# Kernel tuning notes

Measured on AMD Instinct MI355X. Metric: run time of the kernel, lower is better.

The kernel has to match this reference:

```python
import jax, jax.numpy as jnp
import numpy as np

B, T, C = 2, 2048, 1024
H = 16
D = C // H
E = 16
K = 2
THETA = 10000.0
ALPHA = 0.01
EPS = 1e-5


def rmsnorm(x, w):
    ms = jnp.mean(jnp.square(x), axis=-1, keepdims=True)
    return x * jax.lax.rsqrt(ms + EPS) * w


def rope_cos_sin(t_len, dim):
    # matches precompute_freqs_cis: freqs = theta**(-2i/dim), angles = t * freqs
    freqs = 1.0 / THETA ** (jnp.arange(0, dim // 2, dtype=jnp.float32) * 2.0 / dim)
    ang = jnp.arange(t_len, dtype=jnp.float32)[:, None] * freqs[None, :]  # [T, D/2]
    return jnp.cos(ang), jnp.sin(ang)


def apply_rope(x, cos, sin):
    # x: [B,T,H,D]; complex rotation on consecutive pairs (view_as_complex semantics)
    xr = x.reshape(x.shape[:-1] + (D // 2, 2))
    x0, x1 = xr[..., 0], xr[..., 1]
    c = cos[None, :, None, :]
    s = sin[None, :, None, :]
    return jnp.stack([x0 * c - x1 * s, x0 * s + x1 * c], axis=-1).reshape(x.shape)


def mlp(x, wf, bf, wp, bp):
    return jax.nn.silu(x @ wf + bf) @ wp + bp


def setup_inputs() -> dict:
    key = jax.random.key(0)
    ks = jax.random.split(key, 16)
    s = 0.02
    return {
        'x': jax.random.normal(ks[0], (B, T, C), jnp.float32),
        'ln1_w': jax.random.normal(ks[1], (C,), jnp.float32),
        'ln2_w': jax.random.normal(ks[2], (C,), jnp.float32),
        'w_attn': jax.random.normal(ks[3], (C, 3 * C), jnp.float32) * s,
        'b_attn': jnp.zeros((3 * C,), jnp.float32),
        'w_proj': jax.random.normal(ks[4], (C, C), jnp.float32) * s,
        'b_proj': jnp.zeros((C,), jnp.float32),
        'gate_w': jax.random.normal(ks[5], (E, C), jnp.float32) * s,
        'gate_bias': jnp.zeros((E,), jnp.float32),
        'exp_wf': jax.random.normal(ks[6], (E, C, 2 * C), jnp.float32) * s,
        'exp_bf': jnp.zeros((E, 2 * C), jnp.float32),
        'exp_wp': jax.random.normal(ks[7], (E, 2 * C, C), jnp.float32) * s,
        'exp_bp': jnp.zeros((E, C), jnp.float32),
        'sh_wf': jax.random.normal(ks[8], (C, 2 * C), jnp.float32) * s,
        'sh_bf': jnp.zeros((2 * C,), jnp.float32),
        'sh_wp': jax.random.normal(ks[9], (2 * C, C), jnp.float32) * s,
        'sh_bp': jnp.zeros((C,), jnp.float32),
    }


def reference(x, ln1_w, ln2_w, w_attn, b_attn, w_proj, b_proj, gate_w, gate_bias,
              exp_wf, exp_bf, exp_wp, exp_bp, sh_wf, sh_bf, sh_wp, sh_bp):
    # ---- attention sub-block ----
    h = rmsnorm(x, ln1_w)
    qkv = h @ w_attn + b_attn  # [B,T,3C]
    q, k, v = jnp.split(qkv, 3, axis=-1)
    q = q.reshape(B, T, H, D)
    k = k.reshape(B, T, H, D)
    v = v.reshape(B, T, H, D)
    cos, sin = rope_cos_sin(T, D)
    q = apply_rope(q, cos, sin)
    k = apply_rope(k, cos, sin)
    scores = jnp.einsum('bqhd,bkhd->bhqk', q, k) / jnp.sqrt(jnp.float32(D))
    causal = jnp.tril(jnp.ones((T, T), dtype=bool))
    scores = jnp.where(causal, scores, -jnp.inf)
    attn = jax.nn.softmax(scores, axis=-1)
    y = jnp.einsum('bhqk,bkhd->bqhd', attn, v).reshape(B, T, C)
    x = x + y @ w_proj + b_proj
    # ---- MoE sub-block ----
    h = rmsnorm(x, ln2_w).reshape(-1, C)  # [N,C]
    N = h.shape[0]
    logits = h @ gate_w.T
    p = jax.nn.softmax(logits.astype(jnp.float32), axis=-1)  # original_scores [N,E]
    _, idx = jax.lax.top_k(p + gate_bias, K)  # topk on biased scores
    w_sel = jnp.take_along_axis(p, idx, axis=-1)  # weights from unbiased scores [N,K]
    onehot = jax.nn.one_hot(idx, E, dtype=p.dtype)  # [N,K,E]
    w_dense = jnp.sum(onehot * w_sel[..., None], axis=1)  # [N,E] combine weights
    counts = jnp.sum(onehot, axis=(0, 1))  # bincount
    f_i = counts * E / (K * N + 1e-6)
    expert_probs = p.mean(axis=0)
    lb_loss = ALPHA * jnp.sum(f_i * expert_probs)
    out = jnp.zeros_like(h)
    for i in range(E):  # fixed small expert count
        out = out + mlp(h, exp_wf[i], exp_bf[i], exp_wp[i], exp_bp[i]) * w_dense[:, i:i + 1]
    out = out + mlp(h, sh_wf, sh_bf, sh_wp, sh_bp)
    return x + out.reshape(B, T, C), lb_loss
```

## Files before the change

kernel.cpp:

```cpp
#include <hip/hip_runtime.h>

typedef __bf16 bf16x8 __attribute__((ext_vector_type(8)));
typedef short  short8 __attribute__((ext_vector_type(8)));
typedef float  f32x4  __attribute__((ext_vector_type(4)));
typedef unsigned short u16;

#define NTOK 4096
#define TSEQ 2048
#define CDIM 1024
#define NEXP 16

__device__ __forceinline__ u16 f2bf(float f){
  union { float f; unsigned u; } v; v.f = f;
  unsigned r = v.u + 0x7fffu + ((v.u >> 16) & 1u);
  return (u16)(r >> 16);
}
__device__ __forceinline__ float bf2f(u16 u){
  union { unsigned u; float f; } v; v.u = ((unsigned)u) << 16; return v.f;
}

__device__ __forceinline__ f32x4 mfma16(short8 a, short8 b, f32x4 c){
  return __builtin_amdgcn_mfma_f32_16x16x32_bf16(
      __builtin_bit_cast(bf16x8, a), __builtin_bit_cast(bf16x8, b), c, 0, 0, 0);
}

__device__ __forceinline__ void gload_lds16(const void* g, void* l){
  __builtin_amdgcn_global_load_lds((__attribute__((address_space(1))) void*)g,
                                   (__attribute__((address_space(3))) void*)l,
                                   16, 0, 0);
}

__device__ __forceinline__ void tp_body(const float* __restrict__ in, u16* __restrict__ out,
                                        int K, int N, int k0, int n0, u16* lds16, int tid)
{
  int tx = tid & 15;
#pragma unroll
  for (int p = 0; p < 2; ++p) {
    int q = (tid >> 4) + p * 16;
    int k = 2 * q;
    float4 v0 = *(const float4*)(in + (size_t)(k0 + k)     * N + n0 + tx * 4);
    float4 v1 = *(const float4*)(in + (size_t)(k0 + k + 1) * N + n0 + tx * 4);
    const float* a0 = (const float*)&v0;
    const float* a1 = (const float*)&v1;
#pragma unroll
    for (int i = 0; i < 4; ++i) {
      unsigned val = (unsigned)f2bf(a0[i]) | ((unsigned)f2bf(a1[i]) << 16);
      *(unsigned*)&lds16[(tx * 4 + i) * 66 + k] = val;
    }
  }
  __syncthreads();
#pragma unroll
  for (int p = 0; p < 2; ++p) {
    int n = (tid >> 3) + p * 32;
    int k8 = (tid & 7) * 8;
    const unsigned* l32 = (const unsigned*)&lds16[n * 66 + k8];
    uint4 o4;
    o4.x = l32[0]; o4.y = l32[1]; o4.z = l32[2]; o4.w = l32[3];
    *(uint4*)(out + (size_t)(n0 + n) * K + k0 + k8) = o4;
  }
}

__global__ void transpose_wattn_k(const float* __restrict__ in, u16* __restrict__ out)
{
  __shared__ u16 lds16[64 * 66];
  int r = blockIdx.x;
  int n0 = (r % 48) * 64, k0 = (r / 48) * 64;
  tp_body(in, out, 1024, 3072, k0, n0, lds16, threadIdx.x);
}

__global__ void concat_bias_k(const float* __restrict__ exp_bf, const float* __restrict__ sh_bf,
                              const float* __restrict__ exp_bp, const float* __restrict__ sh_bp,
                              float* __restrict__ bf17, float* __restrict__ bp17,
                              int* __restrict__ counts)
{
  int i = blockIdx.x * 256 + threadIdx.x;
  if (i < 16 * 2048) bf17[i] = exp_bf[i];
  else if (i < 17 * 2048) bf17[i] = sh_bf[i - 16 * 2048];
  if (i < 16 * 1024) bp17[i] = exp_bp[i];
  else if (i < 17 * 1024) bp17[i] = sh_bp[i - 16 * 1024];
  if (blockIdx.x == 0 && threadIdx.x <= NEXP)
    counts[threadIdx.x] = (threadIdx.x == NEXP) ? NTOK : 0;
}

__global__ void rmsnorm_k(const float* __restrict__ x, const float* __restrict__ w,
                          u16* __restrict__ ob)
{
  int row = blockIdx.x, tid = threadIdx.x;
  const float4* xr = (const float4*)(x + (size_t)row * CDIM);
  float4 v = xr[tid];
  float ss = v.x*v.x + v.y*v.y + v.z*v.z + v.w*v.w;
  for (int d = 1; d < 64; d <<= 1) ss += __shfl_xor(ss, d);
  __shared__ float wacc[4];
  if ((tid & 63) == 0) wacc[tid >> 6] = ss;
  __syncthreads();
  float tot = wacc[0] + wacc[1] + wacc[2] + wacc[3];
  float scale = rsqrtf(tot * (1.0f / CDIM) + 1e-5f);
  float4 wv = ((const float4*)w)[tid];
  float o0 = v.x * scale * wv.x, o1 = v.y * scale * wv.y;
  float o2 = v.z * scale * wv.z, o3 = v.w * scale * wv.w;
  ushort4 ov; ov.x = f2bf(o0); ov.y = f2bf(o1); ov.z = f2bf(o2); ov.w = f2bf(o3);
  ((ushort4*)(ob + (size_t)row * CDIM))[tid] = ov;
}

__global__ void rmsnorm_gate_k(const float* __restrict__ x2, const float* __restrict__ w,
                               const float* __restrict__ gw, const float* __restrict__ gb,
                               u16* __restrict__ ob,
                               int* __restrict__ route_e, float* __restrict__ route_w,
                               int* __restrict__ counts, float* __restrict__ probs)
{
  int row = blockIdx.x, tid = threadIdx.x;
  __shared__ float hrow[CDIM];
  __shared__ float wacc[4];
  __shared__ float part[16][17];
  __shared__ float sm[16];

  const float4* xr = (const float4*)(x2 + (size_t)row * CDIM);
  float4 v = xr[tid];
  float ss = v.x*v.x + v.y*v.y + v.z*v.z + v.w*v.w;
  for (int d = 1; d < 64; d <<= 1) ss += __shfl_xor(ss, d);
  if ((tid & 63) == 0) wacc[tid >> 6] = ss;
  __syncthreads();
  float tot = wacc[0] + wacc[1] + wacc[2] + wacc[3];
  float scale = rsqrtf(tot * (1.0f / CDIM) + 1e-5f);
  float4 wv = ((const float4*)w)[tid];
  float o0 = v.x * scale * wv.x, o1 = v.y * scale * wv.y;
  float o2 = v.z * scale * wv.z, o3 = v.w * scale * wv.w;
  ((float4*)hrow)[tid] = make_float4(o0, o1, o2, o3);
  ushort4 ov; ov.x = f2bf(o0); ov.y = f2bf(o1); ov.z = f2bf(o2); ov.w = f2bf(o3);
  ((ushort4*)(ob + (size_t)row * CDIM))[tid] = ov;
  __syncthreads();

  int e = tid & 15, seg = tid >> 4;
  const float4* gw4 = (const float4*)(gw + (size_t)e * CDIM + seg * 64);
  const float4* hs4 = (const float4*)(hrow + seg * 64);
  float p = 0.f;
#pragma unroll
  for (int i = 0; i < 16; ++i) {
    float4 gv = gw4[i];
    float4 hv = hs4[i];
    p += hv.x * gv.x;
    p += hv.y * gv.y;
    p += hv.z * gv.z;
    p += hv.w * gv.w;
  }
  part[e][seg] = p;
  __syncthreads();
  if (tid < 16) {
    float lg = 0.f;
    for (int s = 0; s < 16; ++s) lg += part[tid][s];
    sm[tid] = lg;
  }
  __syncthreads();
  if (tid == 0) {
    float mx = sm[0];
    for (int i = 1; i < 16; ++i) mx = fmaxf(mx, sm[i]);
    float ssum = 0.f;
    for (int i = 0; i < 16; ++i) { float pe = expf(sm[i] - mx); sm[i] = pe; ssum += pe; }
    float inv = 1.0f / ssum;
    for (int i = 0; i < 16; ++i) sm[i] *= inv;
    int i1 = -1; float b1 = -1e30f;
    for (int i = 0; i < 16; ++i) { float t = sm[i] + gb[i]; if (t > b1) { b1 = t; i1 = i; } }
    int i2 = -1; float b2 = -1e30f;
    for (int i = 0; i < 16; ++i) { if (i == i1) continue; float t = sm[i] + gb[i]; if (t > b2) { b2 = t; i2 = i; } }
    route_e[2 * row] = i1; route_e[2 * row + 1] = i2;
    route_w[2 * row] = sm[i1]; route_w[2 * row + 1] = sm[i2];
    atomicAdd(&counts[i1], 1); atomicAdd(&counts[i2], 1);
  }
  __syncthreads();
  if (tid < 16) probs[(size_t)row * 16 + tid] = sm[tid];
}

template<int MODE, int SWZ>
__global__ void __launch_bounds__(256, 4)
gemm_bt(const u16* __restrict__ A, int lda,
        const u16* __restrict__ Bt, long long bStrideZ,
        const float* __restrict__ bias, int biasStrideZ,
        void* __restrict__ Cout,
        const float* __restrict__ resid,
        int M, int N, int K,
        const int* __restrict__ counts, const int* __restrict__ offsets,
        const int* __restrict__ tokA, u16* __restrict__ vtp)
{
  int cb, rb, z;
  if (SWZ) {
    int nwg = gridDim.x * gridDim.y * gridDim.z;
    int d = (blockIdx.z * gridDim.y + blockIdx.y) * gridDim.x + blockIdx.x;
    int o = (d & 7) * (nwg >> 3) + (d >> 3);
    cb = o % gridDim.x;
    int t2 = o / gridDim.x;
    rb = t2 % gridDim.y;
    z  = t2 / gridDim.y;
  } else {
    cb = blockIdx.x; rb = blockIdx.y; z = blockIdx.z;
  }

  int mLoc = M, rowBase = 0;
  if (counts) { mLoc = counts[z]; rowBase = offsets[z]; }
  if (rb * 128 >= mLoc) return;

  const u16* Bz = Bt + (size_t)z * bStrideZ;
  const float* bz = bias + (size_t)z * biasStrideZ;

  __shared__ u16 lds_a[2][128 * 32];
  __shared__ u16 lds_b[2][128 * 32];

  int tid = threadIdx.x;
  int lane = tid & 63, wave = tid >> 6;
  int wm = wave >> 1, wn = wave & 1;
  int srow = wave * 16 + (lane >> 2);
  int skel = (lane & 3) * 8;
  int r16 = lane & 15, g8 = (lane >> 4) * 8;

  size_t arow[2];
  int ncol[2];
#pragma unroll
  for (int c = 0; c < 2; ++c) {
    int rloc = rb * 128 + c * 64 + srow;
    if (rloc >= mLoc) rloc = mLoc - 1;
    int grow = rowBase + rloc;
    arow[c] = tokA ? (size_t)tokA[grow] : (size_t)grow;
    ncol[c] = cb * 128 + c * 64 + srow;
  }

  f32x4 acc[4][4] = {};

  auto stage = [&](int kt, int buf){
    int k0 = kt * 32;
#pragma unroll
    for (int c = 0; c < 2; ++c) {
      gload_lds16(A + arow[c] * lda + k0 + skel,
                  (char*)&lds_a[buf][0] + c * 4096 + wave * 1024);
      gload_lds16(Bz + (size_t)ncol[c] * K + k0 + skel,
                  (char*)&lds_b[buf][0] + c * 4096 + wave * 1024);
    }
  };

  int nkt = K >> 5;
  stage(0, 0);
  for (int kt = 0; kt < nkt; ++kt) {
    int buf = kt & 1;
    if (kt + 1 < nkt) {
      stage(kt + 1, buf ^ 1);
      asm volatile("s_waitcnt vmcnt(4)" ::: "memory");
    } else {
      asm volatile("s_waitcnt vmcnt(0)" ::: "memory");
    }
    __builtin_amdgcn_s_barrier();
    short8 af[4], bfr[4];
#pragma unroll
    for (int i = 0; i < 4; ++i) {
      af[i]  = *(const short8*)&lds_a[buf][(wm * 64 + i * 16 + r16) * 32 + g8];
      bfr[i] = *(const short8*)&lds_b[buf][(wn * 64 + i * 16 + r16) * 32 + g8];
    }
#pragma unroll
    for (int i = 0; i < 4; ++i)
#pragma unroll
      for (int j = 0; j < 4; ++j)
        acc[i][j] = mfma16(af[i], bfr[j], acc[i][j]);
    __builtin_amdgcn_s_barrier();
  }

#pragma unroll
  for (int i = 0; i < 4; ++i) {
    int rl0 = rb * 128 + wm * 64 + i * 16 + (lane >> 4) * 4;
#pragma unroll
    for (int j = 0; j < 4; ++j) {
      int col = cb * 128 + wn * 64 + j * 16 + r16;
      float bv = bz[col];
#pragma unroll
      for (int r = 0; r < 4; ++r) {
        int rl = rl0 + r;
        if (rl >= mLoc) continue;
        int grow = rowBase + rl;
        float v = acc[i][j][r] + bv;
        if (MODE == 0) {
          ((float*)Cout)[(size_t)grow * N + col] = v;
        } else if (MODE == 1) {
          ((float*)Cout)[(size_t)grow * N + col] = v + resid[(size_t)grow * N + col];
        } else if (MODE == 2) {
          float s = v * (1.0f / (1.0f + __expf(-v)));
          ((u16*)Cout)[(size_t)grow * N + col] = f2bf(s);
        } else if (MODE == 4) {
          ((u16*)Cout)[(size_t)grow * N + col] = f2bf(v);
        } else {
          if (col < 2048) {
            ((float*)Cout)[(size_t)grow * N + col] = v;
          } else {
            int c10 = col - 2048;
            int h = c10 >> 6, dd = c10 & 63;
            int b = grow >> 11, t = grow & 2047;
            vtp[((size_t)(b * 16 + h) * 64 + dd) * TSEQ + t] = f2bf(v);
          }
        }
      }
    }
  }
}

__global__ void rope_qk_k(const float* __restrict__ qkv,
                          u16* __restrict__ qr, u16* __restrict__ kr)
{
  int flat = blockIdx.x * 256 + threadIdx.x;
  int i = flat & 31;
  int h = (flat >> 5) & 15;
  int n = flat >> 9;
  int b = n >> 11, t = n & 2047;
  const float* row = qkv + (size_t)n * 3072;
  float2 q = *(const float2*)(row + h * 64 + 2 * i);
  float2 k = *(const float2*)(row + 1024 + h * 64 + 2 * i);
  float freq = expf(-(float)i * (2.0f / 64.0f) * 9.210340371976184f);
  float ang = (float)t * freq;
  float sn, cs;
  sincosf(ang, &sn, &cs);
  float q0 = q.x * cs - q.y * sn, q1 = q.x * sn + q.y * cs;
  float k0 = k.x * cs - k.y * sn, k1 = k.x * sn + k.y * cs;
  int bh = b * 16 + h;
  size_t qoff = ((size_t)bh * TSEQ + t) * 64 + 2 * i;
  *(unsigned*)(qr + qoff) = (unsigned)f2bf(q0) | ((unsigned)f2bf(q1) << 16);
  *(unsigned*)(kr + qoff) = (unsigned)f2bf(k0) | ((unsigned)f2bf(k1) << 16);
}

__global__ void __launch_bounds__(512, 4)
attn_tp_k(const u16* __restrict__ qr, const u16* __restrict__ kr,
          const u16* __restrict__ vt, u16* __restrict__ y,
          const float* __restrict__ wProj, const float* __restrict__ shWf,
          const float* __restrict__ shWp,  const float* __restrict__ expWf,
          const float* __restrict__ expWp,
          u16* __restrict__ oProj, u16* __restrict__ oWf17, u16* __restrict__ oWp17)
{
  __shared__ union {
    struct { u16 lK[2][64 * 64]; u16 lV[2][64 * 64]; u16 plds[8][16 * 72]; } a;
    u16 t[2][64 * 66];
  } sm;

  int u = blockIdx.x;
  if (u >= 512) {
    int tid = threadIdx.x;
    int half = tid >> 8, t256 = tid & 255;
    int t = (u - 512) * 2 + half;
    const float* in; u16* out; int K, N, k0, n0;
    if (t < 8192) {
      int z = t >> 9, r = t & 511;
      in = expWf + (size_t)z * 2048 * 1024; out = oWf17 + (size_t)z * 2048 * 1024;
      K = 1024; N = 2048; n0 = (r & 31) * 64; k0 = (r >> 5) * 64;
    } else if (t < 16384) {
      int z = (t - 8192) >> 9, r = (t - 8192) & 511;
      in = expWp + (size_t)z * 2048 * 1024; out = oWp17 + (size_t)z * 2048 * 1024;
      K = 2048; N = 1024; n0 = (r & 15) * 64; k0 = (r >> 4) * 64;
    } else if (t < 16896) {
      int r = t - 16384;
      in = shWf; out = oWf17 + (size_t)16 * 2048 * 1024;
      K = 1024; N = 2048; n0 = (r & 31) * 64; k0 = (r >> 5) * 64;
    } else if (t < 17408) {
      int r = t - 16896;
      in = shWp; out = oWp17 + (size_t)16 * 2048 * 1024;
      K = 2048; N = 1024; n0 = (r & 15) * 64; k0 = (r >> 4) * 64;
    } else {
      int r = t - 17408;
      in = wProj; out = oProj; K = 1024; N = 1024; n0 = (r & 15) * 64; k0 = (r >> 4) * 64;
    }
    tp_body(in, out, K, N, k0, n0, &sm.t[half][0], t256);
    return;
  }

  int j  = u >> 5;
  int bh = u & 31;
  int b = bh >> 4, h = bh & 15;
  int qb = 15 - j;
  int tid = threadIdx.x;
  int wv = tid >> 6, lane = tid & 63;
  int qrow0 = qb * 128 + wv * 16;
  const u16* qbase = qr + (size_t)bh * TSEQ * 64;
  const u16* kbase = kr + (size_t)bh * TSEQ * 64;
  const u16* vbase = vt + (size_t)bh * 64 * TSEQ;

  u16* pw = &sm.a.plds[wv][0];

  int r16 = lane & 15, g = lane >> 4;

  short8 aq0 = *(const short8*)(qbase + (size_t)(qrow0 + r16) * 64 + g * 8);
  short8 aq1 = *(const short8*)(qbase + (size_t)(qrow0 + r16) * 64 + 32 + g * 8);

  int sRow = tid >> 3;
  int sColE = (((tid & 7) * 16) ^ ((sRow & 7) << 4)) >> 1;

  float m[4] = {-1e30f, -1e30f, -1e30f, -1e30f};
  float l[4] = {0.f, 0.f, 0.f, 0.f};
  f32x4 o[4] = {};

  int nt = 2 * qb + 2;

  auto stage = [&](int t, int buf){
    int kp = t * 64;
    gload_lds16(kbase + ((size_t)(kp + sRow) << 6) + sColE,
                (char*)&sm.a.lK[buf][0] + wv * 1024);
    gload_lds16(vbase + (size_t)sRow * TSEQ + kp + sColE,
                (char*)&sm.a.lV[buf][0] + wv * 1024);
  };

  auto compute = [&](int t, int buf){
    int kp = t * 64;
    f32x4 s[4];
    __builtin_amdgcn_s_setprio(1);
#pragma unroll
    for (int st = 0; st < 4; ++st) {
      int rowK = st * 16 + r16;
      int sw = (rowK & 7) << 4;
      short8 kb0 = *(const short8*)((const char*)&sm.a.lK[buf][0] + rowK * 128 + ((g * 16) ^ sw));
      short8 kb1 = *(const short8*)((const char*)&sm.a.lK[buf][0] + rowK * 128 + ((64 + g * 16) ^ sw));
      f32x4 acc = {0.f, 0.f, 0.f, 0.f};
      acc = mfma16(aq0, kb0, acc);
      acc = mfma16(aq1, kb1, acc);
      s[st] = acc;
    }
    __builtin_amdgcn_s_setprio(0);

    float sc[4];
#pragma unroll
    for (int r = 0; r < 4; ++r) {
      int qpos = qrow0 + g * 4 + r;
      float v0 = (kp + r16      <= qpos) ? s[0][r] * 0.125f : -1e30f;
      float v1 = (kp + 16 + r16 <= qpos) ? s[1][r] * 0.125f : -1e30f;
      float v2 = (kp + 32 + r16 <= qpos) ? s[2][r] * 0.125f : -1e30f;
      float v3 = (kp + 48 + r16 <= qpos) ? s[3][r] * 0.125f : -1e30f;
      float mx = fmaxf(fmaxf(v0, v1), fmaxf(v2, v3));
      for (int d = 1; d < 16; d <<= 1) mx = fmaxf(mx, __shfl_xor(mx, d));
      float mnew = fmaxf(m[r], mx);
      float e0 = __expf(v0 - mnew), e1 = __expf(v1 - mnew);
      float e2 = __expf(v2 - mnew), e3 = __expf(v3 - mnew);
      float scale = __expf(m[r] - mnew);
      float rs = (e0 + e1) + (e2 + e3);
      for (int d = 1; d < 16; d <<= 1) rs += __shfl_xor(rs, d);
      l[r] = l[r] * scale + rs;
      m[r] = mnew;
      sc[r] = scale;
      int prow = (g * 4 + r) * 72;
      pw[prow + r16]      = f2bf(e0);
      pw[prow + 16 + r16] = f2bf(e1);
      pw[prow + 32 + r16] = f2bf(e2);
      pw[prow + 48 + r16] = f2bf(e3);
    }
#pragma unroll
    for (int c = 0; c < 4; ++c) {
      f32x4 t4 = o[c];
      t4[0] *= sc[0]; t4[1] *= sc[1]; t4[2] *= sc[2]; t4[3] *= sc[3];
      o[c] = t4;
    }

    short8 pa0 = *(const short8*)&pw[r16 * 72 + g * 8];
    short8 pa1 = *(const short8*)&pw[r16 * 72 + 32 + g * 8];
    __builtin_amdgcn_s_setprio(1);
#pragma unroll
    for (int c = 0; c < 4; ++c) {
      int rowV = c * 16 + r16;
      int sw = (rowV & 7) << 4;
      short8 vb0 = *(const short8*)((const char*)&sm.a.lV[buf][0] + rowV * 128 + ((g * 16) ^ sw));
      short8 vb1 = *(const short8*)((const char*)&sm.a.lV[buf][0] + rowV * 128 + ((64 + g * 16) ^ sw));
      o[c] = mfma16(pa0, vb0, o[c]);
      o[c] = mfma16(pa1, vb1, o[c]);
    }
    __builtin_amdgcn_s_setprio(0);
  };

  stage(0, 0);
  for (int t = 0; t < nt; ++t) {
    int buf = t & 1;
    if (t + 1 < nt) {
      stage(t + 1, buf ^ 1);
      asm volatile("s_waitcnt vmcnt(2)" ::: "memory");
    } else {
      asm volatile("s_waitcnt vmcnt(0)" ::: "memory");
    }
    __builtin_amdgcn_s_barrier();
    compute(t, buf);
    __builtin_amdgcn_s_barrier();
  }

#pragma unroll
  for (int c = 0; c < 4; ++c)
#pragma unroll
    for (int r = 0; r < 4; ++r) {
      int qpos = qrow0 + g * 4 + r;
      float val = o[c][r] / l[r];
      y[((size_t)(b * TSEQ + qpos)) * CDIM + h * 64 + c * 16 + r16] = f2bf(val);
    }
}

__global__ void scan_k(const int* counts, int* offs, int* cursors){
  if (threadIdx.x == 0) {
    int acc = 0;
    for (int e = 0; e < NEXP; ++e) { offs[e] = acc; cursors[e] = acc; acc += counts[e]; }
    offs[NEXP] = acc;
  }
}

__global__ void fill_k(const int* __restrict__ route_e, const float* __restrict__ route_w,
                       int* __restrict__ cursors, int* __restrict__ tok, float* __restrict__ tw,
                       int* __restrict__ inv)
{
  int n = blockIdx.x * 256 + threadIdx.x;
  if (n >= NTOK) return;
  for (int j = 0; j < 2; ++j) {
    int e = route_e[2 * n + j];
    int pos = atomicAdd(&cursors[e], 1);
    tok[pos] = n; tw[pos] = route_w[2 * n + j];
    inv[2 * n + j] = pos;
  }
  tok[2 * NTOK + n] = n;
}

__global__ void combine_k(float* __restrict__ out, const float* __restrict__ x2,
                          const u16* __restrict__ eout,
                          const int* __restrict__ inv, const float* __restrict__ tw)
{
  int n = blockIdx.x, tid = threadIdx.x;
  int p0 = inv[2 * n], p1 = inv[2 * n + 1];
  float w0 = tw[p0], w1 = tw[p1];
  float4 xr = ((const float4*)(x2 + (size_t)n * CDIM))[tid];
  ushort4 es = ((const ushort4*)(eout + (size_t)(2 * NTOK + n) * CDIM))[tid];
  float4 a;
  a.x = xr.x + bf2f(es.x);
  a.y = xr.y + bf2f(es.y);
  a.z = xr.z + bf2f(es.z);
  a.w = xr.w + bf2f(es.w);
  ushort4 e0 = ((const ushort4*)(eout + (size_t)p0 * CDIM))[tid];
  ushort4 e1 = ((const ushort4*)(eout + (size_t)p1 * CDIM))[tid];
  a.x += bf2f(e0.x) * w0 + bf2f(e1.x) * w1;
  a.y += bf2f(e0.y) * w0 + bf2f(e1.y) * w1;
  a.z += bf2f(e0.z) * w0 + bf2f(e1.z) * w1;
  a.w += bf2f(e0.w) * w0 + bf2f(e1.w) * w1;
  ((float4*)(out + (size_t)n * CDIM))[tid] = a;
}

__global__ void lb2_k(const int* __restrict__ counts, const float* __restrict__ probs,
                      float* __restrict__ out)
{
  __shared__ float part[256][16];
  int t = threadIdx.x;
  float acc[16];
#pragma unroll
  for (int e = 0; e < 16; ++e) acc[e] = 0.f;
  for (int n = t; n < NTOK; n += 256) {
    const float4* row = (const float4*)(probs + (size_t)n * 16);
    float4 a0 = row[0], a1 = row[1], a2 = row[2], a3 = row[3];
    acc[0] += a0.x; acc[1] += a0.y; acc[2]  += a0.z; acc[3]  += a0.w;
    acc[4] += a1.x; acc[5] += a1.y; acc[6]  += a1.z; acc[7]  += a1.w;
    acc[8] += a2.x; acc[9] += a2.y; acc[10] += a2.z; acc[11] += a2.w;
    acc[12] += a3.x; acc[13] += a3.y; acc[14] += a3.z; acc[15] += a3.w;
  }
#pragma unroll
  for (int e = 0; e < 16; ++e) part[t][e] = acc[e];
  __syncthreads();
  __shared__ float colsum[16];
  if (t < 16) {
    float s = 0.f;
    for (int i = 0; i < 256; ++i) s += part[i][t];
    colsum[t] = s;
  }
  __syncthreads();
  if (t == 0) {
    float accl = 0.f;
    for (int e = 0; e < NEXP; ++e) {
      float f = (float)counts[e] * (16.0f / (2.0f * (float)NTOK + 1e-6f));
      accl += f * (colsum[e] * (1.0f / (float)NTOK));
    }
    out[0] = 0.01f * accl;
  }
}

extern "C" void kernel_launch(void* const* d_in, const int* in_sizes, int n_in,
                              void* d_out, int out_size, void* d_ws, size_t ws_size,
                              hipStream_t stream)
{
  const float* x      = (const float*)d_in[0];
  const float* ln1_w  = (const float*)d_in[1];
  const float* ln2_w  = (const float*)d_in[2];
  const float* w_attn = (const float*)d_in[3];
  const float* b_attn = (const float*)d_in[4];
  const float* w_proj = (const float*)d_in[5];
  const float* b_proj = (const float*)d_in[6];
  const float* gate_w = (const float*)d_in[7];
  const float* gate_b = (const float*)d_in[8];
  const float* exp_wf = (const float*)d_in[9];
  const float* exp_bf = (const float*)d_in[10];
  const float* exp_wp = (const float*)d_in[11];
  const float* exp_bp = (const float*)d_in[12];
  const float* sh_wf  = (const float*)d_in[13];
  const float* sh_bf  = (const float*)d_in[14];
  const float* sh_wp  = (const float*)d_in[15];
  const float* sh_bp  = (const float*)d_in[16];

  char* ws = (char*)d_ws;
  size_t off = 0;
  auto alloc = [&](size_t b){ size_t r = off; off = (off + b + 255) & ~(size_t)255; return r; };

  size_t oWAttnT = alloc(3072ull * 1024 * 2);
  size_t oWProjT = alloc(1024ull * 1024 * 2);
  size_t oExpWfT = alloc(17ull * 2048 * 1024 * 2);
  size_t oExpWpT = alloc(17ull * 1024 * 2048 * 2);
  size_t oX2     = alloc(4096ull * 1024 * 4);
  size_t oH2B    = alloc(4096ull * 1024 * 2);
  size_t oQKV    = alloc(4096ull * 3072 * 4);
  size_t oQR     = alloc(4096ull * 1024 * 2);
  size_t oKR     = alloc(4096ull * 1024 * 2);
  size_t oVT     = alloc(4096ull * 1024 * 2);
  size_t oH1B    = alloc(4096ull * 1024 * 2);
  size_t oCnt    = alloc(128);
  size_t oOffs   = alloc(128);
  size_t oCurs   = alloc(128);
  size_t oRE     = alloc(8192ull * 4);
  size_t oRW     = alloc(8192ull * 4);
  size_t oTok    = alloc(12288ull * 4);
  size_t oTw     = alloc(8192ull * 4);
  size_t oInv    = alloc(8192ull * 4);
  size_t oProbs  = alloc(4096ull * 16 * 4);
  size_t oBf17   = alloc(17ull * 2048 * 4);
  size_t oBp17   = alloc(17ull * 1024 * 4);

  u16* pWAttnT = (u16*)(ws + oWAttnT);
  u16* pWProjT = (u16*)(ws + oWProjT);
  u16* pWf17   = (u16*)(ws + oExpWfT);
  u16* pWp17   = (u16*)(ws + oExpWpT);
  float* pX2   = (float*)(ws + oX2);
  u16* pH2B    = (u16*)(ws + oH2B);
  float* pQKV  = (float*)(ws + oQKV);
  u16* pHid17  = (u16*)(ws + oQKV);
  u16* pQR     = (u16*)(ws + oQR);
  u16* pKR     = (u16*)(ws + oKR);
  u16* pVT     = (u16*)(ws + oVT);
  u16* pH1B    = (u16*)(ws + oH1B);
  u16* pY      = (u16*)(ws + oH1B);
  u16* pEoutB  = (u16*)(ws + oQR);
  int* pCnt    = (int*)(ws + oCnt);
  int* pOffs   = (int*)(ws + oOffs);
  int* pCurs   = (int*)(ws + oCurs);
  int* pRE     = (int*)(ws + oRE);
  float* pRW   = (float*)(ws + oRW);
  int* pTok    = (int*)(ws + oTok);
  float* pTw   = (float*)(ws + oTw);
  int* pInv    = (int*)(ws + oInv);
  float* pProbs= (float*)(ws + oProbs);
  float* pBf17 = (float*)(ws + oBf17);
  float* pBp17 = (float*)(ws + oBp17);

  transpose_wattn_k<<<768, 256, 0, stream>>>(w_attn, pWAttnT);
  concat_bias_k<<<(17 * 2048 + 255) / 256, 256, 0, stream>>>(exp_bf, sh_bf, exp_bp, sh_bp,
                                                             pBf17, pBp17, pCnt);

  rmsnorm_k<<<NTOK, 256, 0, stream>>>(x, ln1_w, pH1B);

  gemm_bt<5, 1><<<dim3(3072/128, NTOK/128, 1), 256, 0, stream>>>(
      pH1B, 1024, pWAttnT, 0, b_attn, 0, pQKV, nullptr,
      NTOK, 3072, 1024, nullptr, nullptr, nullptr, pVT);

  rope_qk_k<<<(NTOK * 16 * 32) / 256, 256, 0, stream>>>(pQKV, pQR, pKR);

  attn_tp_k<<<512 + 8832, 512, 0, stream>>>(pQR, pKR, pVT, pY,
                                            w_proj, sh_wf, sh_wp, exp_wf, exp_wp,
                                            pWProjT, pWf17, pWp17);

  gemm_bt<1, 1><<<dim3(1024/128, NTOK/128, 1), 256, 0, stream>>>(
      pY, 1024, pWProjT, 0, b_proj, 0, pX2, x,
      NTOK, 1024, 1024, nullptr, nullptr, nullptr, nullptr);

  rmsnorm_gate_k<<<NTOK, 256, 0, stream>>>(pX2, ln2_w, gate_w, gate_b,
                                           pH2B, pRE, pRW, pCnt, pProbs);

  scan_k<<<1, 64, 0, stream>>>(pCnt, pOffs, pCurs);
  fill_k<<<NTOK/256, 256, 0, stream>>>(pRE, pRW, pCurs, pTok, pTw, pInv);
  lb2_k<<<1, 256, 0, stream>>>(pCnt, pProbs, ((float*)d_out) + (size_t)NTOK * CDIM);

  gemm_bt<2, 0><<<dim3(2048/128, NTOK/128, 17), 256, 0, stream>>>(
      pH2B, 1024, pWf17, 2048ll * 1024, pBf17, 2048, pHid17, nullptr,
      NTOK, 2048, 1024, pCnt, pOffs, pTok, nullptr);

  gemm_bt<4, 0><<<dim3(1024/128, NTOK/128, 17), 256, 0, stream>>>(
      pHid17, 2048, pWp17, 2048ll * 1024, pBp17, 1024, pEoutB, nullptr,
      NTOK, 1024, 2048, pCnt, pOffs, nullptr, nullptr);

  combine_k<<<NTOK, 256, 0, stream>>>((float*)d_out, pX2, pEoutB, pInv, pTw);

  (void)in_sizes; (void)n_in; (void)out_size; (void)ws_size;
}
```

Before: 591.0 us.

## Overlap expert down-proj weight transpose with FF GEMM, fuse routing kernels

Moves the transpose/convert of the expert Wp weights out of the attention kernel's tail and into a new fused kernel that also runs the first expert FF GEMM, so the transpose blocks fill idle CUs while the grouped GEMM runs. The scan, fill and load-balance loss kernels are merged into one single-block kernel that uses shared-memory cursors. A dedicated FF GEMM kernel with SiLU epilogue replaces the generic gemm_bt<2> launch. This cuts launches and rebalances work across kernels, but the ff_tp_k grid is large and its early-exit blocks plus the transpose tail may not overlap well. The single-block routing kernel also serialises atomics through one CU.

Result: faster. 555.7 us (median of 2 runs) (-6.0%).

```diff
diff --git a/kernel.cpp b/kernel.cpp
--- a/kernel.cpp
+++ b/kernel.cpp
@@ -297,27 +297,111 @@
   }
 }
 
-__global__ void rope_qk_k(const float* __restrict__ qkv,
-                          u16* __restrict__ qr, u16* __restrict__ kr)
-{
-  int flat = blockIdx.x * 256 + threadIdx.x;
-  int i = flat & 31;
-  int h = (flat >> 5) & 15;
-  int n = flat >> 9;
-  int b = n >> 11, t = n & 2047;
-  const float* row = qkv + (size_t)n * 3072;
-  float2 q = *(const float2*)(row + h * 64 + 2 * i);
-  float2 k = *(const float2*)(row + 1024 + h * 64 + 2 * i);
-  float freq = expf(-(float)i * (2.0f / 64.0f) * 9.210340371976184f);
-  float ang = (float)t * freq;
-  float sn, cs;
-  sincosf(ang, &sn, &cs);
-  float q0 = q.x * cs - q.y * sn, q1 = q.x * sn + q.y * cs;
-  float k0 = k.x * cs - k.y * sn, k1 = k.x * sn + k.y * cs;
-  int bh = b * 16 + h;
-  size_t qoff = ((size_t)bh * TSEQ + t) * 64 + 2 * i;
-  *(unsigned*)(qr + qoff) = (unsigned)f2bf(q0) | ((unsigned)f2bf(q1) << 16);
-  *(unsigned*)(kr + qoff) = (unsigned)f2bf(k0) | ((unsigned)f2bf(k1) << 16);
+__global__ void __launch_bounds__(256, 4)
+ff_tp_k(const u16* __restrict__ A, const u16* __restrict__ Wf17,
+        const float* __restrict__ bf17, u16* __restrict__ hid17,
+        const int* __restrict__ counts, const int* __restrict__ offsets,
+        const int* __restrict__ tokA,
+        const float* __restrict__ expWp, u16* __restrict__ oWp17)
+{
+  __shared__ union {
+    struct { u16 a[2][128 * 32]; u16 b[2][128 * 32]; } g;
+    u16 t[64 * 66];
+  } sm;
+
+  int u = blockIdx.x;
+  if (u >= 8704) {
+    int t = u - 8704;
+    int z = t >> 9, r = t & 511;
+    tp_body(expWp + (size_t)z * 2048 * 1024, oWp17 + (size_t)z * 2048 * 1024,
+            2048, 1024, (r >> 4) * 64, (r & 15) * 64, sm.t, threadIdx.x);
+    return;
+  }
+
+  const int N = 2048, K = 1024, lda = 1024;
+  int cb = u & 15, t2 = u >> 4;
+  int rb = t2 & 31, z = t2 >> 5;
+
+  int mLoc = counts[z], rowBase = offsets[z];
+  if (rb * 128 >= mLoc) return;
+
+  const u16* Bz = Wf17 + (size_t)z * 2048 * 1024;
+  const float* bz = bf17 + (size_t)z * 2048;
+
+  int tid = threadIdx.x;
+  int lane = tid & 63, wave = tid >> 6;
+  int wm = wave >> 1, wn = wave & 1;
+  int srow = wave * 16 + (lane >> 2);
+  int skel = (lane & 3) * 8;
+  int r16 = lane & 15, g8 = (lane >> 4) * 8;
+
+  size_t arow[2];
+  int ncol[2];
+#pragma unroll
+  for (int c = 0; c < 2; ++c) {
+    int rloc = rb * 128 + c * 64 + srow;
+    if (rloc >= mLoc) rloc = mLoc - 1;
+    int grow = rowBase + rloc;
+    arow[c] = (size_t)tokA[grow];
+    ncol[c] = cb * 128 + c * 64 + srow;
+  }
+
+  f32x4 acc[4][4] = {};
+
+  auto stage = [&](int kt, int buf){
+    int k0 = kt * 32;
+#pragma unroll
+    for (int c = 0; c < 2; ++c) {
+      gload_lds16(A + arow[c] * lda + k0 + skel,
+                  (char*)&sm.g.a[buf][0] + c * 4096 + wave * 1024);
+      gload_lds16(Bz + (size_t)ncol[c] * K + k0 + skel,
+                  (char*)&sm.g.b[buf][0] + c * 4096 + wave * 1024);
+    }
+  };
+
+  int nkt = K >> 5;
+  stage(0, 0);
+  for (int kt = 0; kt < nkt; ++kt) {
+    int buf = kt & 1;
+    if (kt + 1 < nkt) {
+      stage(kt + 1, buf ^ 1);
+      asm volatile("s_waitcnt vmcnt(4)" ::: "memory");
+    } else {
+      asm volatile("s_waitcnt vmcnt(0)" ::: "memory");
+    }
+    __builtin_amdgcn_s_barrier();
+    short8 af[4], bfr[4];
+#pragma unroll
+    for (int i = 0; i < 4; ++i) {
+      af[i]  = *(const short8*)&sm.g.a[buf][(wm * 64 + i * 16 + r16) * 32 + g8];
+      bfr[i] = *(const short8*)&sm.g.b[buf][(wn * 64 + i * 16 + r16) * 32 + g8];
+    }
+#pragma unroll
+    for (int i = 0; i < 4; ++i)
+#pragma unroll
+      for (int j = 0; j < 4; ++j)
+        acc[i][j] = mfma16(af[i], bfr[j], acc[i][j]);
+    __builtin_amdgcn_s_barrier();
+  }
+
+#pragma unroll
+  for (int i = 0; i < 4; ++i) {
+    int rl0 = rb * 128 + wm * 64 + i * 16 + (lane >> 4) * 4;
+#pragma unroll
+    for (int j = 0; j < 4; ++j) {
+      int col = cb * 128 + wn * 64 + j * 16 + r16;
+      float bv = bz[col];
+#pragma unroll
+      for (int r = 0; r < 4; ++r) {
+        int rl = rl0 + r;
+        if (rl >= mLoc) continue;
+        int grow = rowBase + rl;
+        float v = acc[i][j][r] + bv;
+        float s = v * (1.0f / (1.0f + __expf(-v)));
+        hid17[(size_t)grow * N + col] = f2bf(s);
+      }
+    }
+  }
 }
 
 __global__ void __launch_bounds__(512, 4)
@@ -325,7 +409,6 @@
           const u16* __restrict__ vt, u16* __restrict__ y,
           const float* __restrict__ wProj, const float* __restrict__ shWf,
           const float* __restrict__ shWp,  const float* __restrict__ expWf,
-          const float* __restrict__ expWp,
           u16* __restrict__ oProj, u16* __restrict__ oWf17, u16* __restrict__ oWp17)
 {
   __shared__ union {
@@ -343,20 +426,16 @@
       int z = t >> 9, r = t & 511;
       in = expWf + (size_t)z * 2048 * 1024; out = oWf17 + (size_t)z * 2048 * 1024;
       K = 1024; N = 2048; n0 = (r & 31) * 64; k0 = (r >> 5) * 64;
-    } else if (t < 16384) {
-      int z = (t - 8192) >> 9, r = (t - 8192) & 511;
-      in = expWp + (size_t)z * 2048 * 1024; out = oWp17 + (size_t)z * 2048 * 1024;
-      K = 2048; N = 1024; n0 = (r & 15) * 64; k0 = (r >> 4) * 64;
-    } else if (t < 16896) {
-      int r = t - 16384;
+    } else if (t < 8704) {
+      int r = t - 8192;
       in = shWf; out = oWf17 + (size_t)16 * 2048 * 1024;
       K = 1024; N = 2048; n0 = (r & 31) * 64; k0 = (r >> 5) * 64;
-    } else if (t < 17408) {
-      int r = t - 16896;
+    } else if (t < 9216) {
+      int r = t - 8704;
       in = shWp; out = oWp17 + (size_t)16 * 2048 * 1024;
       K = 2048; N = 1024; n0 = (r & 15) * 64; k0 = (r >> 4) * 64;
     } else {
-      int r = t - 17408;
+      int r = t - 9216;
       in = wProj; out = oProj; K = 1024; N = 1024; n0 = (r & 15) * 64; k0 = (r >> 4) * 64;
     }
     tp_body(in, out, K, N, k0, n0, &sm.t[half][0], t256);
@@ -486,27 +565,84 @@
     }
 }
 
-__global__ void scan_k(const int* counts, int* offs, int* cursors){
-  if (threadIdx.x == 0) {
+__global__ void rope_qk_k(const float* __restrict__ qkv,
+                          u16* __restrict__ qr, u16* __restrict__ kr)
+{
+  int flat = blockIdx.x * 256 + threadIdx.x;
+  int i = flat & 31;
+  int h = (flat >> 5) & 15;
+  int n = flat >> 9;
+  int b = n >> 11, t = n & 2047;
+  const float* row = qkv + (size_t)n * 3072;
+  float2 q = *(const float2*)(row + h * 64 + 2 * i);
+  float2 k = *(const float2*)(row + 1024 + h * 64 + 2 * i);
+  float freq = expf(-(float)i * (2.0f / 64.0f) * 9.210340371976184f);
+  float ang = (float)t * freq;
+  float sn, cs;
+  sincosf(ang, &sn, &cs);
+  float q0 = q.x * cs - q.y * sn, q1 = q.x * sn + q.y * cs;
+  float k0 = k.x * cs - k.y * sn, k1 = k.x * sn + k.y * cs;
+  int bh = b * 16 + h;
+  size_t qoff = ((size_t)bh * TSEQ + t) * 64 + 2 * i;
+  *(unsigned*)(qr + qoff) = (unsigned)f2bf(q0) | ((unsigned)f2bf(q1) << 16);
+  *(unsigned*)(kr + qoff) = (unsigned)f2bf(k0) | ((unsigned)f2bf(k1) << 16);
+}
+
+__global__ void route_fin_k(const int* __restrict__ route_e, const float* __restrict__ route_w,
+                            const int* __restrict__ counts, int* __restrict__ offs,
+                            int* __restrict__ tok, float* __restrict__ tw, int* __restrict__ inv,
+                            const float* __restrict__ probs, float* __restrict__ loss_out)
+{
+  __shared__ int curs[16];
+  __shared__ float part[256][16];
+  __shared__ float colsum[16];
+  int tid = threadIdx.x;
+  if (tid == 0) {
     int acc = 0;
-    for (int e = 0; e < NEXP; ++e) { offs[e] = acc; cursors[e] = acc; acc += counts[e]; }
+    for (int e = 0; e < NEXP; ++e) { offs[e] = acc; curs[e] = acc; acc += counts[e]; }
     offs[NEXP] = acc;
   }
-}
-
-__global__ void fill_k(const int* __restrict__ route_e, const float* __restrict__ route_w,
-                       int* __restrict__ cursors, int* __restrict__ tok, float* __restrict__ tw,
-                       int* __restrict__ inv)
-{
-  int n = blockIdx.x * 256 + threadIdx.x;
-  if (n >= NTOK) return;
-  for (int j = 0; j < 2; ++j) {
-    int e = route_e[2 * n + j];
-    int pos = atomicAdd(&cursors[e], 1);
-    tok[pos] = n; tw[pos] = route_w[2 * n + j];
-    inv[2 * n + j] = pos;
-  }
-  tok[2 * NTOK + n] = n;
+  __syncthreads();
+  for (int n = tid; n < NTOK; n += 1024) {
+    for (int j = 0; j < 2; ++j) {
+      int e = route_e[2 * n + j];
+      int pos = atomicAdd(&curs[e], 1);
+      tok[pos] = n; tw[pos] = route_w[2 * n + j];
+      inv[2 * n + j] = pos;
+    }
+    tok[2 * NTOK + n] = n;
+  }
+  __syncthreads();
+  if (tid < 256) {
+    float acc[16];
+#pragma unroll
+    for (int e = 0; e < 16; ++e) acc[e] = 0.f;
+    for (int n = tid; n < NTOK; n += 256) {
+      const float4* row = (const float4*)(probs + (size_t)n * 16);
+      float4 a0 = row[0], a1 = row[1], a2 = row[2], a3 = row[3];
+      acc[0] += a0.x; acc[1] += a0.y; acc[2]  += a0.z; acc[3]  += a0.w;
+      acc[4] += a1.x; acc[5] += a1.y; acc[6]  += a1.z; acc[7]  += a1.w;
+      acc[8] += a2.x; acc[9] += a2.y; acc[10] += a2.z; acc[11] += a2.w;
+      acc[12] += a3.x; acc[13] += a3.y; acc[14] += a3.z; acc[15] += a3.w;
+    }
+#pragma unroll
+    for (int e = 0; e < 16; ++e) part[tid][e] = acc[e];
+  }
+  __syncthreads();
+  if (tid < 16) {
+    float s = 0.f;
+    for (int i = 0; i < 256; ++i) s += part[i][tid];
+    colsum[tid] = s;
+  }
+  __syncthreads();
+  if (tid == 0) {
+    float accl = 0.f;
+    for (int e = 0; e < NEXP; ++e) {
+      float f = (float)counts[e] * (16.0f / (2.0f * (float)NTOK + 1e-6f));
+      accl += f * (colsum[e] * (1.0f / (float)NTOK));
+    }
+    loss_out[0] = 0.01f * accl;
+  }
 }
 
 __global__ void combine_k(float* __restrict__ out, const float* __restrict__ x2,
@@ -532,42 +668,6 @@
   ((float4*)(out + (size_t)n * CDIM))[tid] = a;
 }
 
-__global__ void lb2_k(const int* __restrict__ counts, const float* __restrict__ probs,
-                      float* __restrict__ out)
-{
-  __shared__ float part[256][16];
-  int t = threadIdx.x;
-  float acc[16];
-#pragma unroll
-  for (int e = 0; e < 16; ++e) acc[e] = 0.f;
-  for (int n = t; n < NTOK; n += 256) {
-    const float4* row = (const float4*)(probs + (size_t)n * 16);
-    float4 a0 = row[0], a1 = row[1], a2 = row[2], a3 = row[3];
-    acc[0] += a0.x; acc[1] += a0.y; acc[2]  += a0.z; acc[3]  += a0.w;
-    acc[4] += a1.x; acc[5] += a1.y; acc[6]  += a1.z; acc[7]  += a1.w;
-    acc[8] += a2.x; acc[9] += a2.y; acc[10] += a2.z; acc[11] += a2.w;
-    acc[12] += a3.x; acc[13] += a3.y; acc[14] += a3.z; acc[15] += a3.w;
-  }
-#pragma unroll
-  for (int e = 0; e < 16; ++e) part[t][e] = acc[e];
-  __syncthreads();
-  __shared__ float colsum[16];
-  if (t < 16) {
-    float s = 0.f;
-    for (int i = 0; i < 256; ++i) s += part[i][t];
-    colsum[t] = s;
-  }
-  __syncthreads();
-  if (t == 0) {
-    float accl = 0.f;
-    for (int e = 0; e < NEXP; ++e) {
-      float f = (float)counts[e] * (16.0f / (2.0f * (float)NTOK + 1e-6f));
-      accl += f * (colsum[e] * (1.0f / (float)NTOK));
-    }
-    out[0] = 0.01f * accl;
-  }
-}
-
 extern "C" void kernel_launch(void* const* d_in, const int* in_sizes, int n_in,
                               void* d_out, int out_size, void* d_ws, size_t ws_size,
                               hipStream_t stream)
@@ -607,7 +707,6 @@
   size_t oH1B    = alloc(4096ull * 1024 * 2);
   size_t oCnt    = alloc(128);
   size_t oOffs   = alloc(128);
-  size_t oCurs   = alloc(128);
   size_t oRE     = alloc(8192ull * 4);
   size_t oRW     = alloc(8192ull * 4);
   size_t oTok    = alloc(12288ull * 4);
@@ -633,7 +732,6 @@
   u16* pEoutB  = (u16*)(ws + oQR);
   int* pCnt    = (int*)(ws + oCnt);
   int* pOffs   = (int*)(ws + oOffs);
-  int* pCurs   = (int*)(ws + oCurs);
   int* pRE     = (int*)(ws + oRE);
   float* pRW   = (float*)(ws + oRW);
   int* pTok    = (int*)(ws + oTok);
@@ -655,8 +753,8 @@
 
   rope_qk_k<<<(NTOK * 16 * 32) / 256, 256, 0, stream>>>(pQKV, pQR, pKR);
 
-  attn_tp_k<<<512 + 8832, 512, 0, stream>>>(pQR, pKR, pVT, pY,
-                                            w_proj, sh_wf, sh_wp, exp_wf, exp_wp,
+  attn_tp_k<<<512 + 4736, 512, 0, stream>>>(pQR, pKR, pVT, pY,
+                                            w_proj, sh_wf, sh_wp, exp_wf,
                                             pWProjT, pWf17, pWp17);
 
   gemm_bt<1, 1><<<dim3(1024/128, NTOK/128, 1), 256, 0, stream>>>(
@@ -666,13 +764,11 @@
   rmsnorm_gate_k<<<NTOK, 256, 0, stream>>>(pX2, ln2_w, gate_w, gate_b,
                                            pH2B, pRE, pRW, pCnt, pProbs);
 
-  scan_k<<<1, 64, 0, stream>>>(pCnt, pOffs, pCurs);
-  fill_k<<<NTOK/256, 256, 0, stream>>>(pRE, pRW, pCurs, pTok, pTw, pInv);
-  lb2_k<<<1, 256, 0, stream>>>(pCnt, pProbs, ((float*)d_out) + (size_t)NTOK * CDIM);
-
-  gemm_bt<2, 0><<<dim3(2048/128, NTOK/128, 17), 256, 0, stream>>>(
-      pH2B, 1024, pWf17, 2048ll * 1024, pBf17, 2048, pHid17, nullptr,
-      NTOK, 2048, 1024, pCnt, pOffs, pTok, nullptr);
+  route_fin_k<<<1, 1024, 0, stream>>>(pRE, pRW, pCnt, pOffs, pTok, pTw, pInv,
+                                      pProbs, ((float*)d_out) + (size_t)NTOK * CDIM);
+
+  ff_tp_k<<<8704 + 8192, 256, 0, stream>>>(pH2B, pWf17, pBf17, pHid17,
+                                           pCnt, pOffs, pTok, exp_wp, pWp17);
 
   gemm_bt<4, 0><<<dim3(1024/128, NTOK/128, 17), 256, 0, stream>>>(
       pHid17, 2048, pWp17, 2048ll * 1024, pBp17, 1024, pEoutB, nullptr,
```
